# Performance work log

Hardware: AMD Instinct MI355X
Metric: run time of the kernel (lower is better)

## Reference

```python
import jax, jax.numpy as jnp
import numpy as np

NPOINT, NSAMPLE, RADIUS, EPS = 128, 32, 0.4, 1e-5
C_IN, C_MID, C_OUT = 256, 256, 256


def setup_inputs() -> dict:
    key = jax.random.key(0)
    ks = jax.random.split(key, 6)
    B, N = 8, 16384
    xyz = jax.random.uniform(ks[0], (B, N, 3), dtype=jnp.float32)
    feats = jax.random.normal(ks[1], (B, N, C_IN), dtype=jnp.float32)
    # SharedMLP: Conv2d 1x1 (no bias, followed by BN) layers 259->256, 256->256
    w1 = jax.random.normal(ks[2], (C_MID, C_IN + 3), dtype=jnp.float32) * 0.05
    w2 = jax.random.normal(ks[3], (C_OUT, C_MID), dtype=jnp.float32) * 0.05
    gamma1 = jnp.ones((C_MID,), jnp.float32); beta1 = jnp.zeros((C_MID,), jnp.float32)
    mean1 = jnp.zeros((C_MID,), jnp.float32); var1 = jnp.ones((C_MID,), jnp.float32)
    gamma2 = jnp.ones((C_OUT,), jnp.float32); beta2 = jnp.zeros((C_OUT,), jnp.float32)
    mean2 = jnp.zeros((C_OUT,), jnp.float32); var2 = jnp.ones((C_OUT,), jnp.float32)
    return {"xyz": xyz, "proposal_features": feats,
            "w1": w1, "gamma1": gamma1, "beta1": beta1, "mean1": mean1, "var1": var1,
            "w2": w2, "gamma2": gamma2, "beta2": beta2, "mean2": mean2, "var2": var2}


def fps(xyz, npoint):
    # Farthest point sampling, CUDA-kernel-faithful: starts at index 0.
    B, N, _ = xyz.shape
    def step(carry, _):
        dist, far = carry
        centroid = jnp.take_along_axis(xyz, far[:, None, None], axis=1)  # [B,1,3]
        d = jnp.sum((xyz - centroid) ** 2, axis=-1)                      # [B,N]
        dist = jnp.minimum(dist, d)
        return (dist, jnp.argmax(dist, axis=-1).astype(jnp.int32)), far
    init = (jnp.full((B, N), 1e10, xyz.dtype), jnp.zeros((B,), jnp.int32))
    _, inds = jax.lax.scan(step, init, None, length=npoint)
    return inds.T  # [B, npoint]


def ball_query(xyz, new_xyz, radius, nsample):
    # First-nsample-in-order points within radius, padded with the first hit.
    B, N, _ = xyz.shape
    d2 = jnp.sum((new_xyz[:, :, None, :] - xyz[:, None, :, :]) ** 2, axis=-1)  # [B,S,N]
    keys = jnp.where(d2 < radius * radius, jnp.arange(N, dtype=jnp.int32), N)
    idx = -jax.lax.top_k(-keys, nsample)[0]  # smallest indices, ascending
    idx = jnp.where(idx < N, idx, idx[..., :1])  # pad invalid with first hit
    return jnp.clip(idx, 0, N - 1)


def gather_points(pts_bnc, idx):
    # pts_bnc [B,N,C], idx [B,S,K] -> [B,S,K,C]
    B, S, K = idx.shape
    flat = jnp.take_along_axis(pts_bnc, idx.reshape(B, S * K)[:, :, None], axis=1)
    return flat.reshape(B, S, K, pts_bnc.shape[-1])


def bn_relu(x, gamma, beta, mean, var):
    return jax.nn.relu((x - mean) * jax.lax.rsqrt(var + EPS) * gamma + beta)


def reference(xyz, proposal_features, w1, gamma1, beta1, mean1, var1,
              w2, gamma2, beta2, mean2, var2):
    # proposal_features arrives as [B, N, C]; torch module permutes to [B, C, N]
    # (we keep channels-last internally, equivalent math).
    inds = fps(xyz, NPOINT)                                   # [B,128]
    new_xyz = jnp.take_along_axis(xyz, inds[:, :, None], axis=1)  # [B,128,3]
    idx = ball_query(xyz, new_xyz, RADIUS, NSAMPLE)           # [B,128,32]
    g_xyz = gather_points(xyz, idx) - new_xyz[:, :, None, :]  # [B,128,32,3]
    g_feat = gather_points(proposal_features, idx)            # [B,128,32,256]
    x = jnp.concatenate([g_xyz, g_feat], axis=-1)             # [B,128,32,259]
    h = bn_relu(jnp.einsum('bskc,oc->bsko', x, w1), gamma1, beta1, mean1, var1)
    h = bn_relu(jnp.einsum('bskc,oc->bsko', h, w2), gamma2, beta2, mean2, var2)
    new_features = jnp.max(h, axis=2)                         # [B,128,256]
    return jnp.transpose(new_features, (0, 2, 1))             # [B,256,128]
```

## Files before the change

kernel.cpp:

```cpp
#include <hip/hip_runtime.h>
#include <hip/hip_bf16.h>
#include <cstdint>
#include <cstddef>

#define NB      8
#define NPTS    16384
#define NPOINT  128
#define NSAMPLE 32
#define CIN     256
#define CMID    256
#define COUT    256
#define KDIM    259
#define KPAD    288
#define XS_STRIDE 296
#define HS_STRIDE 264

typedef __attribute__((ext_vector_type(8))) short bf16x8;
typedef __attribute__((ext_vector_type(4))) float f32x4;

__device__ __forceinline__ short f2bf(float f) {
  unsigned u = __float_as_uint(f);
  u += 0x7fffu + ((u >> 16) & 1u);
  return (short)(u >> 16);
}

#define FPS_T 1024
#define FPS_W (FPS_T / 64)
#define FPS_P (NPTS / FPS_T)

__global__ __launch_bounds__(FPS_T) __attribute__((amdgpu_waves_per_eu(4, 4)))
void fps_kernel(const float* __restrict__ xyz, int* __restrict__ inds) {
  const int b = blockIdx.x;
  const int t = threadIdx.x;
  const int lane = t & 63, w = t >> 6;
  const float* xb = xyz + (size_t)b * NPTS * 3;

  float px[FPS_P], py[FPS_P], pz[FPS_P], dist[FPS_P];
#pragma unroll
  for (int i = 0; i < FPS_P; ++i) {
    const int j = t + (i << 10);
    px[i] = xb[j * 3 + 0];
    py[i] = xb[j * 3 + 1];
    pz[i] = xb[j * 3 + 2];
    dist[i] = 1e10f;
  }
#pragma unroll
  for (int i = 0; i < FPS_P; ++i) {
    asm volatile("" : "+v"(px[i]), "+v"(py[i]), "+v"(pz[i]));
  }

  __shared__ unsigned long long s_pack[2][FPS_W];
  __shared__ float swx[2][FPS_W], swy[2][FPS_W], swz[2][FPS_W];

  int far = 0;
  float cx = xb[0], cy = xb[1], cz = xb[2];

  for (int it = 0; it < NPOINT; ++it) {
    if (t == 0) inds[b * NPOINT + it] = far;
    float best = -1.0f;
    int bi = t;
#pragma unroll
    for (int i = 0; i < FPS_P; ++i) {
      float dx = __fsub_rn(px[i], cx);
      float dy = __fsub_rn(py[i], cy);
      float dz = __fsub_rn(pz[i], cz);
      float d  = __fadd_rn(__fadd_rn(__fmul_rn(dx, dx), __fmul_rn(dy, dy)), __fmul_rn(dz, dz));
      float dm = fminf(dist[i], d);
      dist[i] = dm;
      if (dm > best) { best = dm; bi = t + (i << 10); }
    }
#pragma unroll
    for (int off = 32; off > 0; off >>= 1) {
      float ov = __shfl_down(best, off, 64);
      int   oi = __shfl_down(bi, off, 64);
      if (ov > best || (ov == best && oi < bi)) { best = ov; bi = oi; }
    }
    const int par = it & 1;
    if (lane == 0) {
      s_pack[par][w] = ((unsigned long long)__float_as_uint(best) << 18)
                     | ((unsigned long long)(unsigned)(NPTS - 1 - bi) << 4)
                     | (unsigned long long)w;
      swx[par][w] = xb[bi * 3 + 0];
      swy[par][w] = xb[bi * 3 + 1];
      swz[par][w] = xb[bi * 3 + 2];
    }
    __syncthreads();
    unsigned long long pm = s_pack[par][lane & 15];
#pragma unroll
    for (int off = 8; off > 0; off >>= 1) {
      unsigned long long o = __shfl_xor(pm, off, 64);
      if (o > pm) pm = o;
    }
    const int wi = (int)(pm & 15ull);
    far = (NPTS - 1) - (int)((pm >> 4) & (unsigned long long)(NPTS - 1));
    cx = swx[par][wi]; cy = swy[par][wi]; cz = swz[par][wi];
  }
}

__global__ __launch_bounds__(256) void ballq_kernel(const float* __restrict__ xyz,
                                                    const int* __restrict__ inds,
                                                    int* __restrict__ idx) {
  const int gw   = (blockIdx.x * 256 + threadIdx.x) >> 6;
  const int lane = threadIdx.x & 63;
  const int b = gw >> 7, s = gw & 127;
  const float* xb = xyz + (size_t)b * NPTS * 3;
  const int ind = inds[b * NPOINT + s];
  const float cx = xb[ind * 3 + 0], cy = xb[ind * 3 + 1], cz = xb[ind * 3 + 2];
  int* o = idx + gw * NSAMPLE;
  const float R2 = (float)(0.4 * 0.4);
  int total = 0;
  int first_hit = 0;
  bool have_first = false;
  for (int base = 0; base < NPTS && total < NSAMPLE; base += 64) {
    const int j = base + lane;
    float dx = __fsub_rn(xb[j * 3 + 0], cx);
    float dy = __fsub_rn(xb[j * 3 + 1], cy);
    float dz = __fsub_rn(xb[j * 3 + 2], cz);
    float d2 = __fadd_rn(__fadd_rn(__fmul_rn(dx, dx), __fmul_rn(dy, dy)), __fmul_rn(dz, dz));
    bool hit = d2 < R2;
    unsigned long long m = __ballot(hit);
    if (!have_first && m) { first_hit = base + (int)__builtin_ctzll(m); have_first = true; }
    int pos = total + (int)__popcll(m & ((1ull << lane) - 1ull));
    if (hit && pos < NSAMPLE) o[pos] = j;
    total += (int)__popcll(m);
  }
  for (int p = total + lane; p < NSAMPLE; p += 64) o[p] = first_hit;
}

__global__ __launch_bounds__(256) void prep_kernel(
    const float* __restrict__ w1, const float* __restrict__ g1, const float* __restrict__ be1,
    const float* __restrict__ m1, const float* __restrict__ v1,
    const float* __restrict__ w2, const float* __restrict__ g2, const float* __restrict__ be2,
    const float* __restrict__ m2, const float* __restrict__ v2,
    short* __restrict__ w1b, short* __restrict__ w2b,
    float* __restrict__ b1, float* __restrict__ b2) {
  int i = blockIdx.x * 256 + threadIdx.x;
  if (i < CMID * KPAD) {
    int oc = i / KPAD, c = i - oc * KPAD;
    float a = g1[oc] * rsqrtf(v1[oc] + 1e-5f);
    float val = (c < KDIM) ? w1[oc * KDIM + c] * a : 0.0f;
    w1b[i] = f2bf(val);
    if (c == 0) b1[oc] = be1[oc] - m1[oc] * a;
  }
  if (i < COUT * CMID) {
    int oc = i >> 8, c = i & 255;
    float a = g2[oc] * rsqrtf(v2[oc] + 1e-5f);
    w2b[i] = f2bf(w2[oc * CMID + c] * a);
    if (c == 0) b2[oc] = be2[oc] - m2[oc] * a;
  }
}

__global__ __launch_bounds__(256) void mlp_kernel(
    const float* __restrict__ xyz, const float* __restrict__ feats,
    const int* __restrict__ inds, const int* __restrict__ idx,
    const short* __restrict__ w1b, const short* __restrict__ w2b,
    const float* __restrict__ b1, const float* __restrict__ b2,
    float* __restrict__ out) {
  const int g   = blockIdx.x;
  const int bb  = g >> 7, s = g & 127;
  const int tid = threadIdx.x;
  const int wave = tid >> 6, lane = tid & 63;
  const int lrow = lane & 15, quad = lane >> 4;

  __shared__ short Xs[32 * XS_STRIDE];
  __shared__ short Hs[32 * HS_STRIDE];
  __shared__ int   sj[NSAMPLE];
  __shared__ float scen[3];

  if (tid < NSAMPLE) sj[tid] = idx[g * NSAMPLE + tid];
  if (tid < 3) {
    int ind = inds[bb * NPOINT + s];
    scen[tid] = xyz[((size_t)bb * NPTS + ind) * 3 + tid];
  }
  __syncthreads();

  for (int e = tid; e < 32 * KPAD; e += 256) {
    int r = e / KPAD, c = e - r * KPAD;
    int j = sj[r];
    float val;
    if (c < 3)          val = xyz[((size_t)bb * NPTS + j) * 3 + c] - scen[c];
    else if (c < KDIM)  val = feats[((size_t)bb * NPTS + j) * CIN + (c - 3)];
    else                val = 0.0f;
    Xs[r * XS_STRIDE + c] = f2bf(val);
  }
  __syncthreads();

  const int nw = wave * 64;
  f32x4 acc[4][2];
#pragma unroll
  for (int nt = 0; nt < 4; ++nt)
#pragma unroll
    for (int mt = 0; mt < 2; ++mt) acc[nt][mt] = (f32x4){0.f, 0.f, 0.f, 0.f};

  for (int ks = 0; ks < 9; ++ks) {
    const int ko = ks * 32 + quad * 8;
    bf16x8 a0 = *(const bf16x8*)(&Xs[lrow * XS_STRIDE + ko]);
    bf16x8 a1 = *(const bf16x8*)(&Xs[(lrow + 16) * XS_STRIDE + ko]);
#pragma unroll
    for (int nt = 0; nt < 4; ++nt) {
      const int oc = nw + nt * 16 + lrow;
      bf16x8 bf = *(const bf16x8*)(w1b + oc * KPAD + ko);
      acc[nt][0] = __builtin_amdgcn_mfma_f32_16x16x32_bf16(a0, bf, acc[nt][0], 0, 0, 0);
      acc[nt][1] = __builtin_amdgcn_mfma_f32_16x16x32_bf16(a1, bf, acc[nt][1], 0, 0, 0);
    }
  }

#pragma unroll
  for (int nt = 0; nt < 4; ++nt) {
    const int oc = nw + nt * 16 + lrow;
    const float bias = b1[oc];
#pragma unroll
    for (int mt = 0; mt < 2; ++mt) {
#pragma unroll
      for (int r = 0; r < 4; ++r) {
        int row = mt * 16 + quad * 4 + r;
        float h = fmaxf(acc[nt][mt][r] + bias, 0.0f);
        Hs[row * HS_STRIDE + oc] = f2bf(h);
      }
    }
  }
  __syncthreads();

#pragma unroll
  for (int nt = 0; nt < 4; ++nt)
#pragma unroll
    for (int mt = 0; mt < 2; ++mt) acc[nt][mt] = (f32x4){0.f, 0.f, 0.f, 0.f};

  for (int ks = 0; ks < 8; ++ks) {
    const int ko = ks * 32 + quad * 8;
    bf16x8 a0 = *(const bf16x8*)(&Hs[lrow * HS_STRIDE + ko]);
    bf16x8 a1 = *(const bf16x8*)(&Hs[(lrow + 16) * HS_STRIDE + ko]);
#pragma unroll
    for (int nt = 0; nt < 4; ++nt) {
      const int oc = nw + nt * 16 + lrow;
      bf16x8 bf = *(const bf16x8*)(w2b + oc * CMID + ko);
      acc[nt][0] = __builtin_amdgcn_mfma_f32_16x16x32_bf16(a0, bf, acc[nt][0], 0, 0, 0);
      acc[nt][1] = __builtin_amdgcn_mfma_f32_16x16x32_bf16(a1, bf, acc[nt][1], 0, 0, 0);
    }
  }

#pragma unroll
  for (int nt = 0; nt < 4; ++nt) {
    const int oc = nw + nt * 16 + lrow;
    const float bias = b2[oc];
    float v = -3.4e38f;
#pragma unroll
    for (int mt = 0; mt < 2; ++mt) {
      f32x4 a = acc[nt][mt];
      v = fmaxf(v, fmaxf(fmaxf(a[0], a[1]), fmaxf(a[2], a[3])));
    }
    v = fmaxf(v + bias, 0.0f);
    v = fmaxf(v, __shfl_xor(v, 16, 64));
    v = fmaxf(v, __shfl_xor(v, 32, 64));
    if (lane < 16) out[((size_t)bb * COUT + oc) * NPOINT + s] = v;
  }
}

extern "C" void kernel_launch(void* const* d_in, const int* in_sizes, int n_in,
                              void* d_out, int out_size, void* d_ws, size_t ws_size,
                              hipStream_t stream) {
  const float* xyz   = (const float*)d_in[0];
  const float* feats = (const float*)d_in[1];
  const float* w1    = (const float*)d_in[2];
  const float* g1    = (const float*)d_in[3];
  const float* be1   = (const float*)d_in[4];
  const float* m1    = (const float*)d_in[5];
  const float* v1    = (const float*)d_in[6];
  const float* w2    = (const float*)d_in[7];
  const float* g2    = (const float*)d_in[8];
  const float* be2   = (const float*)d_in[9];
  const float* m2    = (const float*)d_in[10];
  const float* v2    = (const float*)d_in[11];
  float* out = (float*)d_out;

  char* ws = (char*)d_ws;
  int*   inds = (int*)(ws);
  int*   idx  = (int*)(ws + 4096);
  short* w1b  = (short*)(ws + 135168);
  short* w2b  = (short*)(ws + 282624);
  float* b1   = (float*)(ws + 413696);
  float* b2   = (float*)(ws + 414720);

  prep_kernel<<<288, 256, 0, stream>>>(w1, g1, be1, m1, v1, w2, g2, be2, m2, v2,
                                       w1b, w2b, b1, b2);
  fps_kernel<<<NB, FPS_T, 0, stream>>>(xyz, inds);
  ballq_kernel<<<256, 256, 0, stream>>>(xyz, inds, idx);
  mlp_kernel<<<NB * NPOINT, 256, 0, stream>>>(xyz, feats, inds, idx, w1b, w2b, b1, b2, out);
}
```

Measured before the change: 519.2 us.

## Load FPS points as contiguous float4 chunks and keep distances in LDS

The FPS kernel now gives each thread a contiguous run of 16 points, loaded with vectorized float4 reads, instead of points strided by 1024. The running min-distance array moves from registers into padded shared memory, read and written as float4 every iteration. This is meant to cut register pressure and make the initial loads coalesced. In exchange it adds LDS traffic to every one of the 128 serial iterations, and the changed index mapping alters the order in which ties are broken within a thread.

```diff
diff --git a/kernel.cpp b/kernel.cpp
--- a/kernel.cpp
+++ b/kernel.cpp
@@ -27,6 +27,7 @@
 #define FPS_T 1024
 #define FPS_W (FPS_T / 64)
 #define FPS_P (NPTS / FPS_T)
+#define DIST_STRIDE 20
 
 __global__ __launch_bounds__(FPS_T) __attribute__((amdgpu_waves_per_eu(4, 4)))
 void fps_kernel(const float* __restrict__ xyz, int* __restrict__ inds) {
@@ -35,19 +36,23 @@
   const int lane = t & 63, w = t >> 6;
   const float* xb = xyz + (size_t)b * NPTS * 3;
 
-  float px[FPS_P], py[FPS_P], pz[FPS_P], dist[FPS_P];
-#pragma unroll
-  for (int i = 0; i < FPS_P; ++i) {
-    const int j = t + (i << 10);
-    px[i] = xb[j * 3 + 0];
-    py[i] = xb[j * 3 + 1];
-    pz[i] = xb[j * 3 + 2];
-    dist[i] = 1e10f;
-  }
-#pragma unroll
-  for (int i = 0; i < FPS_P; ++i) {
-    asm volatile("" : "+v"(px[i]), "+v"(py[i]), "+v"(pz[i]));
-  }
+  float c[48];
+  {
+    const float4* src = (const float4*)(xb + (size_t)t * FPS_P * 3);
+#pragma unroll
+    for (int q = 0; q < 12; ++q) {
+      float4 v = src[q];
+      c[q * 4 + 0] = v.x; c[q * 4 + 1] = v.y; c[q * 4 + 2] = v.z; c[q * 4 + 3] = v.w;
+    }
+  }
+#pragma unroll
+  for (int q = 0; q < 48; q += 3)
+    asm volatile("" : "+v"(c[q]), "+v"(c[q + 1]), "+v"(c[q + 2]));
+
+  __shared__ float sdist[FPS_T * DIST_STRIDE];
+  float4* dvec = (float4*)(sdist + t * DIST_STRIDE);
+#pragma unroll
+  for (int q = 0; q < 4; ++q) dvec[q] = make_float4(1e10f, 1e10f, 1e10f, 1e10f);
 
   __shared__ unsigned long long s_pack[2][FPS_W];
   __shared__ float swx[2][FPS_W], swy[2][FPS_W], swz[2][FPS_W];
@@ -58,16 +63,25 @@
   for (int it = 0; it < NPOINT; ++it) {
     if (t == 0) inds[b * NPOINT + it] = far;
     float best = -1.0f;
-    int bi = t;
-#pragma unroll
-    for (int i = 0; i < FPS_P; ++i) {
-      float dx = __fsub_rn(px[i], cx);
-      float dy = __fsub_rn(py[i], cy);
-      float dz = __fsub_rn(pz[i], cz);
-      float d  = __fadd_rn(__fadd_rn(__fmul_rn(dx, dx), __fmul_rn(dy, dy)), __fmul_rn(dz, dz));
-      float dm = fminf(dist[i], d);
-      dist[i] = dm;
-      if (dm > best) { best = dm; bi = t + (i << 10); }
+    int bi = 0;
+#pragma unroll
+    for (int q = 0; q < 4; ++q) {
+      float4 dv = dvec[q];
+      float dm[4];
+#pragma unroll
+      for (int r = 0; r < 4; ++r) {
+        const int i = q * 4 + r;
+        float dx = __fsub_rn(c[3 * i + 0], cx);
+        float dy = __fsub_rn(c[3 * i + 1], cy);
+        float dz = __fsub_rn(c[3 * i + 2], cz);
+        float d  = __fadd_rn(__fadd_rn(__fmul_rn(dx, dx), __fmul_rn(dy, dy)), __fmul_rn(dz, dz));
+        dm[r] = fminf((&dv.x)[r], d);
+      }
+#pragma unroll
+      for (int r = 0; r < 4; ++r) {
+        if (dm[r] > best) { best = dm[r]; bi = t * FPS_P + q * 4 + r; }
+      }
+      dvec[q] = make_float4(dm[0], dm[1], dm[2], dm[3]);
     }
 #pragma unroll
     for (int off = 32; off > 0; off >>= 1) {
```

After: 518.4 us. No clear change (-0.2%).
